# Performance work log

Measured on AMD Instinct MI355X. Metric: run time of the kernel, lower is better.

## Reference

```python
import jax, jax.numpy as jnp
import numpy as np

I, O, R = 64, 64, 896          # input / output / regulatory protein counts
N = I + O + R                  # total GRN size
WARMUP = 25                    # warmup_count


def setup_inputs() -> dict:
    key = jax.random.key(0)
    k1, k2, k3, k4 = jax.random.split(key, 4)
    return {
        "inputs": jax.random.uniform(k1, (16384, I), dtype=jnp.float32),
        "identifiers": jax.random.uniform(k2, (N,), dtype=jnp.float32),
        "enhancers": jax.random.uniform(k3, (N,), dtype=jnp.float32),
        "inhibitors": jax.random.uniform(k4, (N,), dtype=jnp.float32),
        "beta": jnp.full((1,), 2.0, dtype=jnp.float32),
        "delta": jnp.full((1,), 1.0, dtype=jnp.float32),
    }


def _signatures(identifiers, enhancers, inhibitors, beta):
    # sig[j, i] = exp(-beta * |tag_j - id_i|): affinity of protein j regulating protein i.
    enh = jnp.exp(-beta * jnp.abs(enhancers[:, None] - identifiers[None, :]))
    inh = jnp.exp(-beta * jnp.abs(inhibitors[:, None] - identifiers[None, :]))
    # output proteins do not regulate others -> zero their rows
    mask = jnp.ones((N,), dtype=enh.dtype).at[I:I + O].set(0.0)[:, None]
    return enh * mask, inh * mask


def _step(conc, sig_diff, delta):
    # conc: [..., N]; sig_diff = enh_sigs - inh_sigs: [N, N]
    dc = (delta / N) * (conc @ sig_diff)
    new = jnp.maximum(conc + dc, 0.0)
    reg = new[..., I:]                                    # outputs + regulatory
    s = jnp.sum(reg, axis=-1, keepdims=True)
    reg = jnp.where(s > 0, reg / s, reg)                  # renormalize
    return jnp.concatenate([conc[..., :I], reg], axis=-1)  # inputs clamped


def reference(inputs, identifiers, enhancers, inhibitors, beta, delta):
    b, d = beta[0], delta[0]
    enh_s, inh_s = _signatures(identifiers, enhancers, inhibitors, b)
    sig_diff = enh_s - inh_s

    # setup(): uniform initial concentrations; warmup(): shared sequential steps
    conc0 = jnp.full((N,), 1.0 / N, dtype=jnp.float32)
    def warm(c, _):
        return _step(c, sig_diff, d), None
    conc, _ = jax.lax.scan(warm, conc0, None, length=WARMUP)

    # per-sample (batched instead of tf.map_fn): set input concs, one step
    B = inputs.shape[0]
    batch_conc = jnp.concatenate(
        [inputs, jnp.broadcast_to(conc[I:], (B, N - I))], axis=-1)
    new = _step(batch_conc, sig_diff, d)
    return new[..., I:I + O]  # output protein concentrations [B, O]
```

## Files before the change

kernel.cpp:

```cpp
#include <hip/hip_runtime.h>
#include <math.h>

#define NJ 960
#define NSRC 896
#define NWARM 25

typedef unsigned long long u64;
typedef unsigned int u32;

#define RK_O 0u
#define CT_O 896u
#define HD_O 1856u
#define WK_F 8192u
#define BASE_F 69632u

#define TAG_RK 0x524B0001u
#define TAG_CT 0x43540001u
#define TAG_HD 0x48440001u

__device__ __forceinline__ void ast(u64* p, u64 v) {
  __hip_atomic_store(p, v, __ATOMIC_RELAXED, __HIP_MEMORY_SCOPE_AGENT);
}
__device__ __forceinline__ u64 ald(const u64* p) {
  return __hip_atomic_load(p, __ATOMIC_RELAXED, __HIP_MEMORY_SCOPE_AGENT);
}
__device__ __forceinline__ u32 poll32(const u64* p, u32 tag) {
  u64 v = ald(p);
  while ((u32)(v >> 32) != tag) { __builtin_amdgcn_s_sleep(8); v = ald(p); }
  return (u32)v;
}

__global__ __launch_bounds__(256, 1) void front_k(
    const float* __restrict__ ident, const float* __restrict__ enh,
    const float* __restrict__ inh, const float* __restrict__ beta,
    const float* __restrict__ delta, void* __restrict__ wsv) {
  __shared__ float2 SE[16][64];
  __shared__ float2 SI[16][64];
  __shared__ float4 SRCX[NSRC];

  u64* RK = (u64*)wsv + RK_O;
  u64* CT = (u64*)wsv + CT_O;
  u64* HD = (u64*)wsv + HD_O;
  float* Wk = (float*)wsv + WK_F;
  float* base = (float*)wsv + BASE_F;

  const int tid = threadIdx.x;
  const float bb = beta[0];
  const float dN = delta[0] / 1024.0f;

  if (blockIdx.x > 30) {
    const int g2 = (int)(blockIdx.x - 31) * 256 + tid;
    int k = g2 / 120;
    int jb = (g2 % 120) * 8;
    float ek = enh[k], ik = inh[k];
    #pragma unroll
    for (int u = 0; u < 8; ++u) {
      float cj = ident[64 + jb + u];
      Wk[(size_t)k * NJ + jb + u] =
          dN * (expf(-bb * fabsf(ek - cj)) - expf(-bb * fabsf(ik - cj)));
    }
    return;
  }

  if (blockIdx.x > 0) {
    const int g = (int)(blockIdx.x - 1) * 256 + tid;
    const int c8 = g & 7;
    if (g < NSRC * 8) {
      int m = g >> 3;
      float myE = enh[128 + m], myI = inh[128 + m];
      int re = 0, ri = 0;
      for (int i = 112 * c8; i < 112 * c8 + 112; ++i) {
        float ev = enh[128 + i], iv = inh[128 + i];
        re += (ev < myE || (ev == myE && i < m)) ? 1 : 0;
        ri += (iv < myI || (iv == myI && i < m)) ? 1 : 0;
      }
      int p = re | (ri << 16);
      p += __shfl_xor(p, 1); p += __shfl_xor(p, 2); p += __shfl_xor(p, 4);
      if (c8 == 0) ast(&RK[m], ((u64)TAG_RK << 32) | (u32)p);
    }
    {
      int j = g >> 3;
      float cj = ident[64 + j];
      int ce = 0, ci = 0;
      for (int i = 112 * c8; i < 112 * c8 + 112; ++i) {
        ce += (enh[128 + i] <= cj) ? 1 : 0;
        ci += (inh[128 + i] <= cj) ? 1 : 0;
      }
      int p = ce | (ci << 16);
      p += __shfl_xor(p, 1); p += __shfl_xor(p, 2); p += __shfl_xor(p, 4);
      if (c8 == 0) ast(&CT[j], ((u64)TAG_CT << 32) | (u32)p);
    }
    {
      int j = g >> 3;
      float cj = ident[64 + j];
      float h = 0.0f;
      for (int k = 8 * c8; k < 8 * c8 + 8; ++k)
        h += expf(-bb * fabsf(enh[k] - cj)) - expf(-bb * fabsf(inh[k] - cj));
      h += __shfl_xor(h, 1); h += __shfl_xor(h, 2); h += __shfl_xor(h, 4);
      if (c8 == 0)
        ast(&HD[j], ((u64)TAG_HD << 32) |
                    (u64)__float_as_uint(dN * h * (1.0f / 1024.0f)));
    }
    return;
  }

  if (tid >= 64) return;
  const int lane = tid;

  for (int m = lane; m < NSRC; m += 64) {
    float e = enh[128 + m], iv = inh[128 + m];
    SRCX[m] = make_float4(expf(bb * e), expf(-bb * e),
                          expf(bb * iv), expf(-bb * iv));
  }
  #pragma unroll
  for (int u = 0; u < 16; ++u) {
    SE[u][lane] = make_float2(0.f, 0.f);
    SI[u][lane] = make_float2(0.f, 0.f);
  }
  asm volatile("s_waitcnt lgkmcnt(0)" ::: "memory");
  __builtin_amdgcn_sched_barrier(0);

  const int c0l = lane * 15;
  float fmv[15], fpv[15], hdv[15], y[15];
  int cc[15], rr[15];
  #pragma unroll
  for (int s = 0; s < 15; ++s) {
    float cj = ident[64 + c0l + s];
    fmv[s] = expf(-bb * cj); fpv[s] = expf(bb * cj);
    y[s] = 1.0f / 1024.0f;
    rr[s] = 0;
  }
  #pragma unroll
  for (int s = 0; s < 15; ++s) {
    cc[s] = (int)poll32(&CT[c0l + s], TAG_CT);
    hdv[s] = __uint_as_float(poll32(&HD[c0l + s], TAG_HD));
  }
  #pragma unroll
  for (int s = 0; s < 15; ++s) {
    int c = c0l + s;
    if (c >= 64) rr[s] = (int)poll32(&RK[c - 64], TAG_RK);
  }

  for (int t = 0; t <= NWARM; ++t) {
    #pragma unroll
    for (int s = 0; s < 15; ++s) {
      int c = c0l + s;
      if (c >= 64) {
        float4 X = SRCX[c - 64];
        int qE = (rr[s] & 0xFFFF) + 1;
        int qI = ((rr[s] >> 16) & 0xFFFF) + 1;
        SE[qE & 15][qE >> 4] = make_float2(y[s] * X.x, y[s] * X.y);
        SI[qI & 15][qI >> 4] = make_float2(y[s] * X.z, y[s] * X.w);
      }
    }
    asm volatile("s_waitcnt lgkmcnt(0)" ::: "memory");
    __builtin_amdgcn_sched_barrier(0);

    float2 tE = make_float2(0.f, 0.f), tI = make_float2(0.f, 0.f);
    #pragma unroll
    for (int u = 0; u < 16; ++u) {
      float2 a = SE[u][lane], b = SI[u][lane];
      tE.x += a.x; tE.y += a.y; tI.x += b.x; tI.y += b.y;
    }
    float4 inc = make_float4(tE.x, tE.y, tI.x, tI.y);
    float4 tot = inc;
    #pragma unroll
    for (int off = 1; off < 64; off <<= 1) {
      float ox = __shfl_up(inc.x, off, 64);
      float oy = __shfl_up(inc.y, off, 64);
      float oz = __shfl_up(inc.z, off, 64);
      float ow = __shfl_up(inc.w, off, 64);
      if (lane >= off) { inc.x += ox; inc.y += oy; inc.z += oz; inc.w += ow; }
    }
    float TEy = __shfl(inc.y, 63, 64);
    float TIy = __shfl(inc.w, 63, 64);
    float2 pe = make_float2(inc.x - tot.x, inc.y - tot.y);
    float2 pi = make_float2(inc.z - tot.z, inc.w - tot.w);

    #pragma unroll
    for (int u = 0; u < 16; ++u) {
      float2 a = SE[u][lane], b = SI[u][lane];
      pe.x += a.x; pe.y += a.y; pi.x += b.x; pi.y += b.y;
      if (lane * 16 + u <= NSRC) { SE[u][lane] = pe; SI[u][lane] = pi; }
    }
    asm volatile("s_waitcnt lgkmcnt(0)" ::: "memory");
    __builtin_amdgcn_sched_barrier(0);

    float nv[15]; float psum = 0.0f;
    #pragma unroll
    for (int s = 0; s < 15; ++s) {
      int cE = cc[s] & 0xFFFF, cI = (cc[s] >> 16) & 0xFFFF;
      float2 AE = SE[cE & 15][cE >> 4];
      float2 AI = SI[cI & 15][cI >> 4];
      float dot = fmv[s] * AE.x + fpv[s] * (TEy - AE.y)
                - fmv[s] * AI.x - fpv[s] * (TIy - AI.y);
      float pre = y[s] + dN * dot;
      if (t < NWARM) {
        nv[s] = fmaxf(pre + hdv[s], 0.0f);
        psum += nv[s];
      } else {
        base[c0l + s] = pre;
      }
    }
    if (t < NWARM) {
      #pragma unroll
      for (int off = 32; off >= 1; off >>= 1) psum += __shfl_xor(psum, off);
      float invs = (psum > 0.0f) ? 1.0f / psum : 1.0f;
      #pragma unroll
      for (int s = 0; s < 15; ++s) y[s] = nv[s] * invs;
    }
  }
}

__global__ __launch_bounds__(512) void batch_k(const float* __restrict__ inp,
                                               const float* __restrict__ ws,
                                               float* __restrict__ out) {
  __shared__ float At[64][36];
  __shared__ float Wl[16][512];
  __shared__ float bch[NJ];

  const int tid = threadIdx.x;
  const int colg = tid & 63;
  const int rowg = tid >> 6;
  const size_t rowbase = (size_t)blockIdx.x * 32;
  const float* __restrict__ Wk = ws + WK_F;

  {
    int r = tid >> 4, c4 = (tid & 15) * 4;
    float4 f4 = *(const float4*)(inp + (rowbase + r) * 64 + c4);
    At[c4 + 0][r] = f4.x; At[c4 + 1][r] = f4.y;
    At[c4 + 2][r] = f4.z; At[c4 + 3][r] = f4.w;
  }
  if (tid < 240) {
    float4 b4 = *(const float4*)(ws + BASE_F + 4 * tid);
    bch[4 * tid + 0] = b4.x; bch[4 * tid + 1] = b4.y;
    bch[4 * tid + 2] = b4.z; bch[4 * tid + 3] = b4.w;
  }

  float acc[4][8];
  float rs[4] = {0.f, 0.f, 0.f, 0.f};

  #pragma unroll 1
  for (int ch = 0; ch < 2; ++ch) {
    const int c0 = ch ? 0 : 512;

    #pragma unroll
    for (int r = 0; r < 4; ++r)
      #pragma unroll
      for (int c = 0; c < 8; ++c) acc[r][c] = 0.0f;

    #pragma unroll 1
    for (int s = 0; s < 4; ++s) {
      __syncthreads();
      #pragma unroll
      for (int i = 0; i < 4; ++i) {
        int fi = tid + i * 512;
        int kk = fi >> 7;
        int c4 = (fi & 127) * 4;
        int j = c0 + c4;
        float4 v = make_float4(0.f, 0.f, 0.f, 0.f);
        if (j < NJ)
          v = *(const float4*)(Wk + (size_t)(16 * s + kk) * NJ + j);
        *(float4*)&Wl[kk][c4] = v;
      }
      __syncthreads();
      #pragma unroll
      for (int kk = 0; kk < 16; ++kk) {
        float4 av = *(const float4*)&At[16 * s + kk][rowg * 4];
        float4 w0 = *(const float4*)&Wl[kk][colg * 4];
        float4 w1 = *(const float4*)&Wl[kk][256 + colg * 4];
        float a_[4] = {av.x, av.y, av.z, av.w};
        float w_[8] = {w0.x, w0.y, w0.z, w0.w, w1.x, w1.y, w1.z, w1.w};
        #pragma unroll
        for (int r = 0; r < 4; ++r)
          #pragma unroll
          for (int c = 0; c < 8; ++c)
            acc[r][c] = fmaf(a_[r], w_[c], acc[r][c]);
      }
    }

    #pragma unroll
    for (int c = 0; c < 8; ++c) {
      int cl = (c < 4) ? (colg * 4 + c) : (256 + colg * 4 + (c - 4));
      int j = c0 + cl;
      float bv = (j < NJ) ? bch[j] : -1.0e30f;
      #pragma unroll
      for (int r = 0; r < 4; ++r)
        rs[r] += fmaxf(acc[r][c] + bv, 0.0f);
    }
  }

  #pragma unroll
  for (int r = 0; r < 4; ++r) {
    float v = rs[r];
    #pragma unroll
    for (int off = 32; off >= 1; off >>= 1) v += __shfl_xor(v, off);
    rs[r] = v;
  }
  if (colg < 16) {
    #pragma unroll
    for (int r = 0; r < 4; ++r) {
      float inv = (rs[r] > 0.0f) ? 1.0f / rs[r] : 1.0f;
      float* op = out + (rowbase + rowg * 4 + r) * 64 + colg * 4;
      float4 o;
      o.x = fmaxf(acc[r][0] + bch[colg * 4 + 0], 0.0f) * inv;
      o.y = fmaxf(acc[r][1] + bch[colg * 4 + 1], 0.0f) * inv;
      o.z = fmaxf(acc[r][2] + bch[colg * 4 + 2], 0.0f) * inv;
      o.w = fmaxf(acc[r][3] + bch[colg * 4 + 3], 0.0f) * inv;
      *(float4*)op = o;
    }
  }
}

extern "C" void kernel_launch(void* const* d_in, const int* in_sizes, int n_in,
                              void* d_out, int out_size, void* d_ws, size_t ws_size,
                              hipStream_t stream) {
  const float* inp   = (const float*)d_in[0];
  const float* ident = (const float*)d_in[1];
  const float* enh   = (const float*)d_in[2];
  const float* inh   = (const float*)d_in[3];
  const float* beta  = (const float*)d_in[4];
  const float* delta = (const float*)d_in[5];

  hipLaunchKernelGGL(front_k, dim3(61), dim3(256), 0, stream,
                     ident, enh, inh, beta, delta, d_ws);
  hipLaunchKernelGGL(batch_k, dim3(512), dim3(512), 0, stream,
                     inp, (const float*)d_ws, (float*)d_out);
}
```

Baseline: 185.3 us.

## Spread warmup recurrence across a full 512-thread block instead of one wavefront

The sequential 25-step warmup previously ran on a single 64-lane wavefront, each lane handling 15 columns. It now uses 8 wavefronts, two columns per thread, with a two-level prefix scan (wave shuffles plus per-wave totals in LDS) and block-wide syncs. Normalisation is deferred to the next step through per-wave partial sums. Helper blocks are resized to 512 threads so the grid shrinks from 61 to 31 blocks. This cuts per-step serial work on the critical path, at the cost of several __syncthreads per iteration.

Measured after the change: 173.8 us. 1.07x faster.

```diff
diff --git a/kernel.cpp b/kernel.cpp
--- a/kernel.cpp
+++ b/kernel.cpp
@@ -30,13 +30,15 @@
   return (u32)v;
 }
 
-__global__ __launch_bounds__(256, 1) void front_k(
+__global__ __launch_bounds__(512, 1) void front_k(
     const float* __restrict__ ident, const float* __restrict__ enh,
     const float* __restrict__ inh, const float* __restrict__ beta,
     const float* __restrict__ delta, void* __restrict__ wsv) {
-  __shared__ float2 SE[16][64];
-  __shared__ float2 SI[16][64];
-  __shared__ float4 SRCX[NSRC];
+  __shared__ float2 scanE[1024];
+  __shared__ float2 scanI[1024];
+  __shared__ float yl[NJ];
+  __shared__ float ssw[8];
+  __shared__ float4 wtot[8];
 
   u64* RK = (u64*)wsv + RK_O;
   u64* CT = (u64*)wsv + CT_O;
@@ -48,8 +50,8 @@
   const float bb = beta[0];
   const float dN = delta[0] / 1024.0f;
 
-  if (blockIdx.x > 30) {
-    const int g2 = (int)(blockIdx.x - 31) * 256 + tid;
+  if (blockIdx.x >= 16) {
+    const int g2 = (int)(blockIdx.x - 16) * 512 + tid;
     int k = g2 / 120;
     int jb = (g2 % 120) * 8;
     float ek = enh[k], ik = inh[k];
@@ -62,8 +64,8 @@
     return;
   }
 
-  if (blockIdx.x > 0) {
-    const int g = (int)(blockIdx.x - 1) * 256 + tid;
+  if (blockIdx.x >= 1) {
+    const int g = (int)(blockIdx.x - 1) * 512 + tid;
     const int c8 = g & 7;
     if (g < NSRC * 8) {
       int m = g >> 3;
@@ -104,66 +106,64 @@
     return;
   }
 
-  if (tid >= 64) return;
-  const int lane = tid;
-
-  for (int m = lane; m < NSRC; m += 64) {
-    float e = enh[128 + m], iv = inh[128 + m];
-    SRCX[m] = make_float4(expf(bb * e), expf(-bb * e),
-                          expf(bb * iv), expf(-bb * iv));
-  }
-  #pragma unroll
-  for (int u = 0; u < 16; ++u) {
-    SE[u][lane] = make_float2(0.f, 0.f);
-    SI[u][lane] = make_float2(0.f, 0.f);
-  }
-  asm volatile("s_waitcnt lgkmcnt(0)" ::: "memory");
-  __builtin_amdgcn_sched_barrier(0);
-
-  const int c0l = lane * 15;
-  float fmv[15], fpv[15], hdv[15], y[15];
-  int cc[15], rr[15];
-  #pragma unroll
-  for (int s = 0; s < 15; ++s) {
-    float cj = ident[64 + c0l + s];
-    fmv[s] = expf(-bb * cj); fpv[s] = expf(bb * cj);
-    y[s] = 1.0f / 1024.0f;
-    rr[s] = 0;
-  }
-  #pragma unroll
-  for (int s = 0; s < 15; ++s) {
-    cc[s] = (int)poll32(&CT[c0l + s], TAG_CT);
-    hdv[s] = __uint_as_float(poll32(&HD[c0l + s], TAG_HD));
-  }
-  #pragma unroll
-  for (int s = 0; s < 15; ++s) {
-    int c = c0l + s;
-    if (c >= 64) rr[s] = (int)poll32(&RK[c - 64], TAG_RK);
-  }
+  const int lane = tid & 63, wvid = tid >> 6;
+  const int p0 = 2 * tid;
+  const int j0 = 2 * tid;
+  const bool hasCol = tid < 480;
+  const bool hasSrc = tid < 448;
+
+  scanE[p0] = make_float2(0.f, 0.f); scanE[p0 + 1] = make_float2(0.f, 0.f);
+  scanI[p0] = make_float2(0.f, 0.f); scanI[p0 + 1] = make_float2(0.f, 0.f);
+  if (hasCol) { yl[j0] = 1.0f / 1024.0f; yl[j0 + 1] = 1.0f / 1024.0f; }
+  if (tid < 8) ssw[tid] = 0.125f;
+
+  float fmv[2], fpv[2], hdv[2];
+  int cc[2] = {0, 0};
+  if (hasCol) {
+    #pragma unroll
+    for (int s = 0; s < 2; ++s) {
+      float cj = ident[64 + j0 + s];
+      fmv[s] = expf(-bb * cj); fpv[s] = expf(bb * cj);
+      cc[s] = (int)poll32(&CT[j0 + s], TAG_CT);
+      hdv[s] = __uint_as_float(poll32(&HD[j0 + s], TAG_HD));
+    }
+  }
+  float4 X[2];
+  int rr[2] = {0, 0};
+  if (hasSrc) {
+    #pragma unroll
+    for (int s = 0; s < 2; ++s) {
+      int m = j0 + s;
+      float e = enh[128 + m], iv = inh[128 + m];
+      X[s] = make_float4(expf(bb * e), expf(-bb * e),
+                         expf(bb * iv), expf(-bb * iv));
+      rr[s] = (int)poll32(&RK[m], TAG_RK);
+    }
+  }
+  float nv[2] = {1.0f / 1024.0f, 1.0f / 1024.0f};
+  __syncthreads();
 
   for (int t = 0; t <= NWARM; ++t) {
-    #pragma unroll
-    for (int s = 0; s < 15; ++s) {
-      int c = c0l + s;
-      if (c >= 64) {
-        float4 X = SRCX[c - 64];
-        int qE = (rr[s] & 0xFFFF) + 1;
-        int qI = ((rr[s] >> 16) & 0xFFFF) + 1;
-        SE[qE & 15][qE >> 4] = make_float2(y[s] * X.x, y[s] * X.y);
-        SI[qI & 15][qI >> 4] = make_float2(y[s] * X.z, y[s] * X.w);
-      }
-    }
-    asm volatile("s_waitcnt lgkmcnt(0)" ::: "memory");
-    __builtin_amdgcn_sched_barrier(0);
-
-    float2 tE = make_float2(0.f, 0.f), tI = make_float2(0.f, 0.f);
-    #pragma unroll
-    for (int u = 0; u < 16; ++u) {
-      float2 a = SE[u][lane], b = SI[u][lane];
-      tE.x += a.x; tE.y += a.y; tI.x += b.x; tI.y += b.y;
-    }
-    float4 inc = make_float4(tE.x, tE.y, tI.x, tI.y);
-    float4 tot = inc;
+    float ssum = ssw[0] + ssw[1] + ssw[2] + ssw[3]
+               + ssw[4] + ssw[5] + ssw[6] + ssw[7];
+    float inv = (ssum > 0.0f) ? 1.0f / ssum : 1.0f;
+
+    if (hasSrc) {
+      #pragma unroll
+      for (int s = 0; s < 2; ++s) {
+        float ym = yl[64 + j0 + s] * inv;
+        scanE[(rr[s] & 0xFFFF) + 1] = make_float2(ym * X[s].x, ym * X[s].y);
+        scanI[((rr[s] >> 16) & 0xFFFF) + 1] =
+            make_float2(ym * X[s].z, ym * X[s].w);
+      }
+    }
+    __syncthreads();
+
+    float2 e0 = scanE[p0], e1v = scanE[p0 + 1];
+    float2 i0 = scanI[p0], i1v = scanI[p0 + 1];
+    float4 tot = make_float4(e0.x + e1v.x, e0.y + e1v.y,
+                             i0.x + i1v.x, i0.y + i1v.y);
+    float4 inc = tot;
     #pragma unroll
     for (int off = 1; off < 64; off <<= 1) {
       float ox = __shfl_up(inc.x, off, 64);
@@ -172,42 +172,50 @@
       float ow = __shfl_up(inc.w, off, 64);
       if (lane >= off) { inc.x += ox; inc.y += oy; inc.z += oz; inc.w += ow; }
     }
-    float TEy = __shfl(inc.y, 63, 64);
-    float TIy = __shfl(inc.w, 63, 64);
-    float2 pe = make_float2(inc.x - tot.x, inc.y - tot.y);
-    float2 pi = make_float2(inc.z - tot.z, inc.w - tot.w);
-
-    #pragma unroll
-    for (int u = 0; u < 16; ++u) {
-      float2 a = SE[u][lane], b = SI[u][lane];
-      pe.x += a.x; pe.y += a.y; pi.x += b.x; pi.y += b.y;
-      if (lane * 16 + u <= NSRC) { SE[u][lane] = pe; SI[u][lane] = pi; }
-    }
-    asm volatile("s_waitcnt lgkmcnt(0)" ::: "memory");
-    __builtin_amdgcn_sched_barrier(0);
-
-    float nv[15]; float psum = 0.0f;
-    #pragma unroll
-    for (int s = 0; s < 15; ++s) {
-      int cE = cc[s] & 0xFFFF, cI = (cc[s] >> 16) & 0xFFFF;
-      float2 AE = SE[cE & 15][cE >> 4];
-      float2 AI = SI[cI & 15][cI >> 4];
-      float dot = fmv[s] * AE.x + fpv[s] * (TEy - AE.y)
-                - fmv[s] * AI.x - fpv[s] * (TIy - AI.y);
-      float pre = y[s] + dN * dot;
-      if (t < NWARM) {
-        nv[s] = fmaxf(pre + hdv[s], 0.0f);
-        psum += nv[s];
-      } else {
-        base[c0l + s] = pre;
+    if (lane == 63) wtot[wvid] = inc;
+    __syncthreads();
+
+    float4 exc = make_float4(inc.x - tot.x, inc.y - tot.y,
+                             inc.z - tot.z, inc.w - tot.w);
+    float4 tsum = make_float4(0.f, 0.f, 0.f, 0.f);
+    #pragma unroll
+    for (int w = 0; w < 8; ++w) {
+      float4 p = wtot[w];
+      if (w < wvid) { exc.x += p.x; exc.y += p.y; exc.z += p.z; exc.w += p.w; }
+      tsum.x += p.x; tsum.y += p.y; tsum.z += p.z; tsum.w += p.w;
+    }
+    float2 pe0 = make_float2(exc.x + e0.x, exc.y + e0.y);
+    float2 pe1 = make_float2(pe0.x + e1v.x, pe0.y + e1v.y);
+    float2 pi0 = make_float2(exc.z + i0.x, exc.w + i0.y);
+    float2 pi1 = make_float2(pi0.x + i1v.x, pi0.y + i1v.y);
+    if (p0 <= NSRC) { scanE[p0] = pe0; scanI[p0] = pi0; }
+    if (p0 + 1 <= NSRC) { scanE[p0 + 1] = pe1; scanI[p0 + 1] = pi1; }
+    __syncthreads();
+
+    float psum = 0.0f;
+    if (hasCol) {
+      #pragma unroll
+      for (int s = 0; s < 2; ++s) {
+        float y_own = nv[s] * inv;
+        int cE = cc[s] & 0xFFFF, cI = (cc[s] >> 16) & 0xFFFF;
+        float2 AE = scanE[cE], AI = scanI[cI];
+        float dot = fmv[s] * AE.x + fpv[s] * (tsum.y - AE.y)
+                  - fmv[s] * AI.x - fpv[s] * (tsum.w - AI.y);
+        float pre = y_own + dN * dot;
+        if (t < NWARM) {
+          nv[s] = fmaxf(pre + hdv[s], 0.0f);
+          psum += nv[s];
+        } else {
+          base[j0 + s] = pre;
+        }
       }
     }
     if (t < NWARM) {
       #pragma unroll
       for (int off = 32; off >= 1; off >>= 1) psum += __shfl_xor(psum, off);
-      float invs = (psum > 0.0f) ? 1.0f / psum : 1.0f;
-      #pragma unroll
-      for (int s = 0; s < 15; ++s) y[s] = nv[s] * invs;
+      if (lane == 0) ssw[wvid] = psum;
+      if (hasCol) { yl[j0] = nv[0]; yl[j0 + 1] = nv[1]; }
+      __syncthreads();
     }
   }
 }
@@ -322,7 +330,7 @@
   const float* beta  = (const float*)d_in[4];
   const float* delta = (const float*)d_in[5];
 
-  hipLaunchKernelGGL(front_k, dim3(61), dim3(256), 0, stream,
+  hipLaunchKernelGGL(front_k, dim3(31), dim3(512), 0, stream,
                      ident, enh, inh, beta, delta, d_ws);
   hipLaunchKernelGGL(batch_k, dim3(512), dim3(512), 0, stream,
                      inp, (const float*)d_ws, (float*)d_out);
```
